# Performance work log

Hardware: AMD Instinct MI355X
Metric: run time of the kernel (lower is better)

## Reference

```python
import jax, jax.numpy as jnp
import numpy as np

HEADS = 16


def setup_inputs() -> dict:
    key = jax.random.key(0)
    ks = jax.random.split(key, 5)
    n, s, d = 2, 2048, 1024
    return {
        "x": jax.random.normal(ks[0], (n, s, d), dtype=jnp.float32),
        "Wqkv": jax.random.normal(ks[1], (3 * d, d), dtype=jnp.float32) * (d ** -0.5),
        "bqkv": jax.random.normal(ks[2], (3 * d,), dtype=jnp.float32) * 0.02,
        "Wd": jax.random.normal(ks[3], (d, d), dtype=jnp.float32) * (d ** -0.5),
        "bd": jax.random.normal(ks[4], (d,), dtype=jnp.float32) * 0.02,
        "mask": 1,
    }


def reference(x, Wqkv, bqkv, Wd, bd, mask):
    n, s, d = x.shape
    h = HEADS
    hd = d // h
    qkv = x @ Wqkv.T + bqkv  # [n, s, 3d]
    q, k, v = jnp.split(qkv, 3, axis=-1)
    # [n, h, s, hd]
    q = q.reshape(n, s, h, hd).transpose(0, 2, 1, 3)
    k = k.reshape(n, s, h, hd).transpose(0, 2, 1, 3)
    v = v.reshape(n, s, h, hd).transpose(0, 2, 1, 3)
    scores = jnp.einsum("bhqd,bhkd->bhqk", q, k)
    if mask:
        causal = jnp.triu(jnp.ones((s, s), dtype=bool), k=1)
        scores = jnp.where(causal, -jnp.inf, scores)
    attn = jax.nn.softmax(scores / jnp.sqrt(jnp.float32(hd)), axis=-1)
    out = jnp.einsum("bhqk,bhkd->bhqd", attn, v)
    out = out.transpose(0, 2, 1, 3).reshape(n, s, d)
    return out @ Wd.T + bd
```

## Files before the change

kernel.cpp:

```cpp
#include <hip/hip_runtime.h>
#include <hip/hip_bf16.h>
#include <cstdint>
#include <cstddef>


typedef __attribute__((ext_vector_type(8))) short bf8_t;
typedef __attribute__((ext_vector_type(4))) float f4_t;

__device__ __forceinline__ unsigned short f2bf(float f) {
    union { float f; unsigned int u; } v; v.f = f;
    unsigned int u = v.u + 0x7FFFu + ((v.u >> 16) & 1u);
    return (unsigned short)(u >> 16);
}
__device__ __forceinline__ float bf2f(unsigned short s) {
    union { unsigned int u; float f; } v; v.u = ((unsigned int)s) << 16;
    return v.f;
}

__device__ __forceinline__ void gl_lds16(const void* g, void* l) {
    __builtin_amdgcn_global_load_lds(
        (const __attribute__((address_space(1))) unsigned int*)g,
        (__attribute__((address_space(3))) unsigned int*)l,
        16, 0, 0);
}

__global__ void cvt_kernel(const float* __restrict__ x,    unsigned short* __restrict__ xb,
                           const float* __restrict__ wq,   unsigned short* __restrict__ wqb,
                           const float* __restrict__ wd,   unsigned short* __restrict__ wdb) {
    int i = blockIdx.x * blockDim.x + threadIdx.x;
    const float* src; unsigned short* dst; int off;
    if (i < 1048576)       { src = x;  dst = xb;  off = i; }
    else if (i < 1835008)  { src = wq; dst = wqb; off = i - 1048576; }
    else                   { src = wd; dst = wdb; off = i - 1835008; }
    float4 f = ((const float4*)src)[off];
    ushort4 o;
    o.x = f2bf(f.x); o.y = f2bf(f.y); o.z = f2bf(f.z); o.w = f2bf(f.w);
    ((ushort4*)dst)[off] = o;
}

template<int MODE, int TM>
__device__ __forceinline__ void gemm_body(
    const unsigned short* __restrict__ A,
    const unsigned short* __restrict__ W,
    const float* __restrict__ bias,
    float* __restrict__ outf,
    unsigned short* __restrict__ qb,
    unsigned short* __restrict__ kb,
    unsigned short* __restrict__ vtb,
    int K, int Nn)
{
    constexpr int HM = TM / 2;
    constexpr int MB = HM / 16;
    constexpr int AI = TM / 32;
    constexpr int SSTG = (TM + 128) * 64;
    constexpr int SMEM = (MODE == 0 && SSTG < 128 * 136) ? 128 * 136 : SSTG;

    __shared__ unsigned short smem[SMEM];
    unsigned short* As = smem;
    unsigned short* Bs = smem + TM * 64;

    const int tid  = threadIdx.x;
    const int lane = tid & 63;
    const int w    = tid >> 6;
    const int wm   = w & 1;
    const int wn   = w >> 1;
    const int quad = lane >> 4;
    const int l16  = lane & 15;
    const int m0   = blockIdx.y * TM;
    const int n0   = blockIdx.x * 128;

    const int lrow = lane >> 3;
    const int lcol = ((lane & 7) ^ lrow) << 3;

    f4_t acc[MB][4];
    {
        f4_t z = {0.f, 0.f, 0.f, 0.f};
        #pragma unroll
        for (int i = 0; i < MB; ++i)
            #pragma unroll
            for (int j = 0; j < 4; ++j) acc[i][j] = z;
    }

    const unsigned short* Agp = A + (size_t)(m0 + w * (TM / 4) + lrow) * K + lcol;
    const unsigned short* Bgp = W + (size_t)(n0 + w * 32 + lrow) * K + lcol;
    unsigned short* lAp = &As[(w * (TM / 4)) * 64];
    unsigned short* lBp = &Bs[(w * 32) * 64];

    for (int kk = 0; kk < K; kk += 64) {
        __syncthreads();
        #pragma unroll
        for (int i = 0; i < AI; ++i)
            gl_lds16(Agp + (size_t)(i * 8) * K + kk, lAp + i * 8 * 64);
        #pragma unroll
        for (int i = 0; i < 4; ++i)
            gl_lds16(Bgp + (size_t)(i * 8) * K + kk, lBp + i * 8 * 64);
        __syncthreads();

        const int sw = l16 & 7;
        #pragma unroll
        for (int ks = 0; ks < 2; ++ks) {
            bf8_t af[MB], bfr[4];
            #pragma unroll
            for (int mb = 0; mb < MB; ++mb)
                af[mb] = *(const bf8_t*)&As[(wm * HM + mb * 16 + l16) * 64 + ((((ks << 2) | quad) ^ sw) << 3)];
            #pragma unroll
            for (int nb = 0; nb < 4; ++nb)
                bfr[nb] = *(const bf8_t*)&Bs[(wn * 64 + nb * 16 + l16) * 64 + ((((ks << 2) | quad) ^ sw) << 3)];
            #pragma unroll
            for (int mb = 0; mb < MB; ++mb)
                #pragma unroll
                for (int nb = 0; nb < 4; ++nb)
                    acc[mb][nb] = __builtin_amdgcn_mfma_f32_16x16x32_bf16(af[mb], bfr[nb], acc[mb][nb], 0, 0, 0);
        }
    }

    if (MODE == 0 && n0 >= 2048) {
        unsigned short* T = smem;
        __syncthreads();
        #pragma unroll
        for (int nb = 0; nb < 4; ++nb) {
            const int colL = wn * 64 + nb * 16 + l16;
            const float bc = bias[n0 + colL];
            #pragma unroll
            for (int mb = 0; mb < MB; ++mb) {
                const int rowL = wm * HM + mb * 16 + quad * 4;
                uint2 p;
                p.x = (unsigned int)f2bf(acc[mb][nb][0] + bc) |
                      ((unsigned int)f2bf(acc[mb][nb][1] + bc) << 16);
                p.y = (unsigned int)f2bf(acc[mb][nb][2] + bc) |
                      ((unsigned int)f2bf(acc[mb][nb][3] + bc) << 16);
                *(uint2*)&T[colL * 136 + rowL] = p;
            }
        }
        __syncthreads();
        const int trow  = tid >> 1;
        const int thalf = (tid & 1) << 6;
        const int head  = ((n0 - 2048) >> 6) + (trow >> 6);
        const int hdi   = trow & 63;
        const int bh    = ((m0 >> 11) << 4) + head;
        const int sq0   = (m0 & 2047) + thalf;
        unsigned short* dst = vtb + ((size_t)bh * 64 + hdi) * 2048 + sq0;
        const unsigned short* srcT = &T[trow * 136 + thalf];
        #pragma unroll
        for (int j = 0; j < 8; ++j)
            *(float4*)(dst + j * 8) = *(const float4*)(srcT + j * 8);
        return;
    }

    #pragma unroll
    for (int nb = 0; nb < 4; ++nb) {
        const int col = n0 + wn * 64 + nb * 16 + l16;
        const float bc = bias[col];
        const int within = col & 1023;
        const int head   = within >> 6;
        const int hdi    = within & 63;
        const bool isQ   = (col < 1024);
        #pragma unroll
        for (int mb = 0; mb < MB; ++mb) {
            #pragma unroll
            for (int r = 0; r < 4; ++r) {
                const int row = m0 + wm * HM + mb * 16 + quad * 4 + r;
                const float v = acc[mb][nb][r] + bc;
                if (MODE == 0) {
                    const int b  = row >> 11;
                    const int sq = row & 2047;
                    const int bh = b * 16 + head;
                    const unsigned short bv = f2bf(v);
                    if (isQ) qb[((size_t)bh * 2048 + sq) * 64 + hdi] = bv;
                    else     kb[((size_t)bh * 2048 + sq) * 64 + hdi] = bv;
                } else {
                    outf[(size_t)row * Nn + col] = v;
                }
            }
        }
    }
}

__global__ __launch_bounds__(256, 2) void qkv_gemm(
    const unsigned short* __restrict__ A, const unsigned short* __restrict__ W,
    const float* __restrict__ bias, unsigned short* __restrict__ qb,
    unsigned short* __restrict__ kb, unsigned short* __restrict__ vtb, int K, int Nn)
{
    gemm_body<0, 128>(A, W, bias, nullptr, qb, kb, vtb, K, Nn);
}

__global__ __launch_bounds__(256, 2) void proj_gemm(
    const unsigned short* __restrict__ A, const unsigned short* __restrict__ W,
    const float* __restrict__ bias, float* __restrict__ outf, int K, int Nn)
{
    gemm_body<1, 64>(A, W, bias, outf, nullptr, nullptr, nullptr, K, Nn);
}

__global__ __launch_bounds__(256, 4) void attn_kernel(
    const unsigned short* __restrict__ qg,
    const unsigned short* __restrict__ kg,
    const unsigned short* __restrict__ vg,
    unsigned short* __restrict__ ao,
    unsigned short* __restrict__ pO,
    float* __restrict__ pL)
{
    __shared__ unsigned short Ks[2][4096];
    __shared__ unsigned short Vs[2][4096];
    __shared__ unsigned short Ps[4096];

    const int tid  = threadIdx.x;
    const int lane = tid & 63;
    const int w    = tid >> 6;
    const int quad = lane >> 4;
    const int l16  = lane & 15;
    const int bx   = blockIdx.x;
    const int bh   = ((bx & 7) << 2) | ((bx >> 3) & 3);
    const int h    = (bx >> 5) & 1;
    const int jj   = bx >> 6;
    const int qtBig   = 31 - jj;
    const int qtSmall = jj;
    const int b    = bh >> 4;
    const int head = bh & 15;
    const int p0len = 32 - jj;
    const int t0 = h ? 17 : 0;
    const int t1 = h ? 33 : 17;

    const unsigned short* Qp = qg + (size_t)bh * 2048 * 64;
    const unsigned short* Kp = kg + (size_t)bh * 2048 * 64;
    const unsigned short* Vp = vg + (size_t)bh * 64 * 2048;

    const int srow = lane >> 3;
    const int scol = ((lane & 7) ^ srow) << 3;
    const unsigned short* kga = Kp + (size_t)(w * 16 + srow) * 64 + scol;
    const unsigned short* vga = Vp + (size_t)(w * 16 + srow) * 2048 + scol;
    const int sw = l16 & 7;

    auto stageKV = [&](int kt, int buf) {
        const int sk0 = kt << 6;
        gl_lds16(kga + (size_t)sk0 * 64,       &Ks[buf][w * 16 * 64]);
        gl_lds16(kga + (size_t)sk0 * 64 + 512, &Ks[buf][(w * 16 + 8) * 64]);
        gl_lds16(vga + sk0,                    &Vs[buf][w * 16 * 64]);
        gl_lds16(vga + sk0 + 8 * 2048,         &Vs[buf][(w * 16 + 8) * 64]);
    };

    bf8_t bones;
    {
        const short one = (l16 == 0) ? (short)0x3F80 : (short)0;
        #pragma unroll
        for (int j = 0; j < 8; ++j) bones[j] = one;
    }

    f4_t oacc[4];
    f4_t lacc;
    {
        f4_t z = {0.f, 0.f, 0.f, 0.f};
        #pragma unroll
        for (int j = 0; j < 4; ++j) oacc[j] = z;
        lacc = z;
    }

    bf8_t aq[2];
    {
        const int qt_init = (t0 >= p0len) ? qtSmall : qtBig;
        const size_t qrow = (size_t)(qt_init * 64 + w * 16 + l16) * 64;
        aq[0] = *(const bf8_t*)(Qp + qrow + quad * 8);
        aq[1] = *(const bf8_t*)(Qp + qrow + 32 + quad * 8);
    }

    auto flushPartial = [&]() {
        const int tb = (h << 9) + (bh << 4) + jj;
        unsigned short* po = pO + (size_t)tb * 4096;
        #pragma unroll
        for (int r = 0; r < 4; ++r) {
            const int row = w * 16 + quad * 4 + r;
            #pragma unroll
            for (int nb = 0; nb < 4; ++nb)
                po[row * 64 + nb * 16 + l16] = f2bf(oacc[nb][r]);
            if (l16 == 0) pL[tb * 64 + row] = lacc[r];
        }
    };

    {
        const int kt0 = (t0 >= p0len) ? (t0 - p0len) : t0;
        stageKV(kt0, t0 & 1);
    }

    for (int t = t0; t < t1; ++t) {
        const int buf = t & 1;
        __syncthreads();

        if (t + 1 < t1) {
            const int t2 = t + 1;
            stageKV((t2 >= p0len) ? (t2 - p0len) : t2, t2 & 1);
        }

        if (t == p0len) {
            flushPartial();
            f4_t z = {0.f, 0.f, 0.f, 0.f};
            #pragma unroll
            for (int j = 0; j < 4; ++j) oacc[j] = z;
            lacc = z;
            const size_t qrow = (size_t)(qtSmall * 64 + w * 16 + l16) * 64;
            aq[0] = *(const bf8_t*)(Qp + qrow + quad * 8);
            aq[1] = *(const bf8_t*)(Qp + qrow + 32 + quad * 8);
        }

        const bool ph1 = (t >= p0len);
        const int  kt  = ph1 ? (t - p0len) : t;
        const int  qtc = ph1 ? qtSmall : qtBig;
        const bool diag = (kt == qtc);

        f4_t sacc[4];
        {
            f4_t z = {0.f, 0.f, 0.f, 0.f};
            #pragma unroll
            for (int j = 0; j < 4; ++j) sacc[j] = z;
        }
        __builtin_amdgcn_s_setprio(1);
        #pragma unroll
        for (int ks = 0; ks < 2; ++ks) {
            #pragma unroll
            for (int nb = 0; nb < 4; ++nb) {
                bf8_t bk = *(const bf8_t*)&Ks[buf][(nb * 16 + l16) * 64 + ((((ks << 2) | quad) ^ sw) << 3)];
                sacc[nb] = __builtin_amdgcn_mfma_f32_16x16x32_bf16(aq[ks], bk, sacc[nb], 0, 0, 0);
            }
        }
        __builtin_amdgcn_s_setprio(0);

        if (!diag) {
            #pragma unroll
            for (int r = 0; r < 4; ++r) {
                const int rloc = (w << 4) + (quad << 2) + r;
                const int rk = rloc & 7;
                #pragma unroll
                for (int nb = 0; nb < 4; ++nb) {
                    union { float f; unsigned int u; } pv;
                    pv.f = exp2f(fmaf(sacc[nb][r], 0.18033688f, -20.197731f));
                    Ps[rloc * 64 + ((((nb << 1) | (l16 >> 3)) ^ rk) << 3) + (l16 & 7)] =
                        (unsigned short)(pv.u >> 16);
                }
            }
        } else {
            #pragma unroll
            for (int r = 0; r < 4; ++r) {
                const int rloc = (w << 4) + (quad << 2) + r;
                const int rk = rloc & 7;
                #pragma unroll
                for (int nb = 0; nb < 4; ++nb) {
                    float e = fmaf(sacc[nb][r], 0.18033688f, -20.197731f);
                    if (nb * 16 + l16 > rloc) e = -1e30f;
                    union { float f; unsigned int u; } pv;
                    pv.f = exp2f(e);
                    Ps[rloc * 64 + ((((nb << 1) | (l16 >> 3)) ^ rk) << 3) + (l16 & 7)] =
                        (unsigned short)(pv.u >> 16);
                }
            }
        }

        __builtin_amdgcn_s_setprio(1);
        #pragma unroll
        for (int ks = 0; ks < 2; ++ks) {
            bf8_t ap = *(const bf8_t*)&Ps[(w * 16 + l16) * 64 + ((((ks << 2) | quad) ^ sw) << 3)];
            #pragma unroll
            for (int nb = 0; nb < 4; ++nb) {
                bf8_t bv = *(const bf8_t*)&Vs[buf][(nb * 16 + l16) * 64 + ((((ks << 2) | quad) ^ sw) << 3)];
                oacc[nb] = __builtin_amdgcn_mfma_f32_16x16x32_bf16(ap, bv, oacc[nb], 0, 0, 0);
            }
            lacc = __builtin_amdgcn_mfma_f32_16x16x32_bf16(ap, bones, lacc, 0, 0, 0);
        }
        __builtin_amdgcn_s_setprio(0);
    }

    if (!h) {
        flushPartial();
    } else {
        #pragma unroll
        for (int r = 0; r < 4; ++r) {
            const float lsum = __shfl(lacc[r], lane & 48);
            const float rl = 1.f / lsum;
            const int sq = qtSmall * 64 + (w << 4) + (quad << 2) + r;
            #pragma unroll
            for (int nb = 0; nb < 4; ++nb) {
                const int dcol = head * 64 + nb * 16 + l16;
                ao[((size_t)(b * 2048 + sq)) * 1024 + dcol] = f2bf(oacc[nb][r] * rl);
            }
        }
    }
}

__global__ void merge_kernel(const unsigned short* __restrict__ pO,
                             const float* __restrict__ pL,
                             unsigned short* __restrict__ ao) {
    const int blk  = blockIdx.x;
    const int bh   = blk >> 4;
    const int jj   = blk & 15;
    const int b    = bh >> 4;
    const int head = bh & 15;
    const int qt   = 31 - jj;
    const int row  = threadIdx.x >> 2;
    const int c0   = (threadIdx.x & 3) << 4;

    const float l = pL[blk * 64 + row] + pL[(512 + blk) * 64 + row];
    const float rl = 1.f / l;
    const unsigned short* p0 = pO + (size_t)blk * 4096 + row * 64 + c0;
    const unsigned short* p1 = pO + (size_t)(512 + blk) * 4096 + row * 64 + c0;
    unsigned short* dst = ao + ((size_t)(b * 2048 + qt * 64 + row)) * 1024 + head * 64 + c0;
    #pragma unroll
    for (int j = 0; j < 16; ++j)
        dst[j] = f2bf((bf2f(p0[j]) + bf2f(p1[j])) * rl);
}

extern "C" void kernel_launch(void* const* d_in, const int* in_sizes, int n_in,
                              void* d_out, int out_size, void* d_ws, size_t ws_size,
                              hipStream_t stream) {
    const float* x    = (const float*)d_in[0];
    const float* Wqkv = (const float*)d_in[1];
    const float* bqkv = (const float*)d_in[2];
    const float* Wd   = (const float*)d_in[3];
    const float* bd   = (const float*)d_in[4];
    float* out = (float*)d_out;

    char* ws = (char*)d_ws;
    unsigned short* xb    = (unsigned short*)(ws);
    unsigned short* wqkvb = (unsigned short*)(ws + 8388608);
    unsigned short* wdb   = (unsigned short*)(ws + 14680064);
    unsigned short* qb2   = (unsigned short*)(ws + 16777216);
    unsigned short* kb2   = (unsigned short*)(ws + 25165824);
    unsigned short* vtb   = (unsigned short*)(ws + 33554432);
    unsigned short* pO    = (unsigned short*)(ws + 41943040);
    float*          pL    = (float*)(ws + 50331648);
    unsigned short* ao    = xb;

    cvt_kernel<<<8192, 256, 0, stream>>>(x, xb, Wqkv, wqkvb, Wd, wdb);

    qkv_gemm<<<dim3(24, 32), 256, 0, stream>>>(
        xb, wqkvb, bqkv, qb2, kb2, vtb, 1024, 3072);

    attn_kernel<<<1024, 256, 0, stream>>>(qb2, kb2, vtb, ao, pO, pL);

    merge_kernel<<<512, 256, 0, stream>>>(pO, pL, ao);

    proj_gemm<<<dim3(8, 64), 256, 0, stream>>>(
        ao, wdb, bd, out, 1024, 1024);
}
```

Baseline: 175.0 us.

## Replace split-KV balanced attention with one block per query tile, drop merge

Each of the 1024 attention blocks used to pair a long and a short causal query tile and split the combined key range into two halves, writing bf16 partials that a separate merge kernel combined. Now each block owns one query tile (qt = 31 - bx>>5) and loops over keys 0..qt, normalizing and writing output directly. This removes the merge launch and the partial-result traffic. In exchange, per-block work becomes imbalanced (1 to 32 key tiles), with the heaviest tiles scheduled first to soften the tail.

```diff
diff --git a/kernel.cpp b/kernel.cpp
--- a/kernel.cpp
+++ b/kernel.cpp
@@ -195,9 +195,7 @@
     const unsigned short* __restrict__ qg,
     const unsigned short* __restrict__ kg,
     const unsigned short* __restrict__ vg,
-    unsigned short* __restrict__ ao,
-    unsigned short* __restrict__ pO,
-    float* __restrict__ pL)
+    unsigned short* __restrict__ ao)
 {
     __shared__ unsigned short Ks[2][4096];
     __shared__ unsigned short Vs[2][4096];
@@ -210,15 +208,9 @@
     const int l16  = lane & 15;
     const int bx   = blockIdx.x;
     const int bh   = ((bx & 7) << 2) | ((bx >> 3) & 3);
-    const int h    = (bx >> 5) & 1;
-    const int jj   = bx >> 6;
-    const int qtBig   = 31 - jj;
-    const int qtSmall = jj;
+    const int qt   = 31 - (bx >> 5);
     const int b    = bh >> 4;
     const int head = bh & 15;
-    const int p0len = 32 - jj;
-    const int t0 = h ? 17 : 0;
-    const int t1 = h ? 33 : 17;
 
     const unsigned short* Qp = qg + (size_t)bh * 2048 * 64;
     const unsigned short* Kp = kg + (size_t)bh * 2048 * 64;
@@ -256,54 +248,21 @@
 
     bf8_t aq[2];
     {
-        const int qt_init = (t0 >= p0len) ? qtSmall : qtBig;
-        const size_t qrow = (size_t)(qt_init * 64 + w * 16 + l16) * 64;
+        const size_t qrow = (size_t)(qt * 64 + w * 16 + l16) * 64;
         aq[0] = *(const bf8_t*)(Qp + qrow + quad * 8);
         aq[1] = *(const bf8_t*)(Qp + qrow + 32 + quad * 8);
     }
 
-    auto flushPartial = [&]() {
-        const int tb = (h << 9) + (bh << 4) + jj;
-        unsigned short* po = pO + (size_t)tb * 4096;
-        #pragma unroll
-        for (int r = 0; r < 4; ++r) {
-            const int row = w * 16 + quad * 4 + r;
-            #pragma unroll
-            for (int nb = 0; nb < 4; ++nb)
-                po[row * 64 + nb * 16 + l16] = f2bf(oacc[nb][r]);
-            if (l16 == 0) pL[tb * 64 + row] = lacc[r];
-        }
-    };
-
-    {
-        const int kt0 = (t0 >= p0len) ? (t0 - p0len) : t0;
-        stageKV(kt0, t0 & 1);
-    }
-
-    for (int t = t0; t < t1; ++t) {
+    stageKV(0, 0);
+
+    for (int t = 0; t <= qt; ++t) {
         const int buf = t & 1;
         __syncthreads();
 
-        if (t + 1 < t1) {
-            const int t2 = t + 1;
-            stageKV((t2 >= p0len) ? (t2 - p0len) : t2, t2 & 1);
-        }
-
-        if (t == p0len) {
-            flushPartial();
-            f4_t z = {0.f, 0.f, 0.f, 0.f};
-            #pragma unroll
-            for (int j = 0; j < 4; ++j) oacc[j] = z;
-            lacc = z;
-            const size_t qrow = (size_t)(qtSmall * 64 + w * 16 + l16) * 64;
-            aq[0] = *(const bf8_t*)(Qp + qrow + quad * 8);
-            aq[1] = *(const bf8_t*)(Qp + qrow + 32 + quad * 8);
-        }
-
-        const bool ph1 = (t >= p0len);
-        const int  kt  = ph1 ? (t - p0len) : t;
-        const int  qtc = ph1 ? qtSmall : qtBig;
-        const bool diag = (kt == qtc);
+        if (t < qt)
+            stageKV(t + 1, (t + 1) & 1);
+
+        const bool diag = (t == qt);
 
         f4_t sacc[4];
         {
@@ -366,43 +325,17 @@
         __builtin_amdgcn_s_setprio(0);
     }
 
-    if (!h) {
-        flushPartial();
-    } else {
-        #pragma unroll
-        for (int r = 0; r < 4; ++r) {
-            const float lsum = __shfl(lacc[r], lane & 48);
-            const float rl = 1.f / lsum;
-            const int sq = qtSmall * 64 + (w << 4) + (quad << 2) + r;
-            #pragma unroll
-            for (int nb = 0; nb < 4; ++nb) {
-                const int dcol = head * 64 + nb * 16 + l16;
-                ao[((size_t)(b * 2048 + sq)) * 1024 + dcol] = f2bf(oacc[nb][r] * rl);
-            }
-        }
-    }
-}
-
-__global__ void merge_kernel(const unsigned short* __restrict__ pO,
-                             const float* __restrict__ pL,
-                             unsigned short* __restrict__ ao) {
-    const int blk  = blockIdx.x;
-    const int bh   = blk >> 4;
-    const int jj   = blk & 15;
-    const int b    = bh >> 4;
-    const int head = bh & 15;
-    const int qt   = 31 - jj;
-    const int row  = threadIdx.x >> 2;
-    const int c0   = (threadIdx.x & 3) << 4;
-
-    const float l = pL[blk * 64 + row] + pL[(512 + blk) * 64 + row];
-    const float rl = 1.f / l;
-    const unsigned short* p0 = pO + (size_t)blk * 4096 + row * 64 + c0;
-    const unsigned short* p1 = pO + (size_t)(512 + blk) * 4096 + row * 64 + c0;
-    unsigned short* dst = ao + ((size_t)(b * 2048 + qt * 64 + row)) * 1024 + head * 64 + c0;
     #pragma unroll
-    for (int j = 0; j < 16; ++j)
-        dst[j] = f2bf((bf2f(p0[j]) + bf2f(p1[j])) * rl);
+    for (int r = 0; r < 4; ++r) {
+        const float lsum = __shfl(lacc[r], lane & 48);
+        const float rl = 1.f / lsum;
+        const int sq = qt * 64 + (w << 4) + (quad << 2) + r;
+        #pragma unroll
+        for (int nb = 0; nb < 4; ++nb) {
+            const int dcol = head * 64 + nb * 16 + l16;
+            ao[((size_t)(b * 2048 + sq)) * 1024 + dcol] = f2bf(oacc[nb][r] * rl);
+        }
+    }
 }
 
 extern "C" void kernel_launch(void* const* d_in, const int* in_sizes, int n_in,
@@ -422,8 +355,6 @@
     unsigned short* qb2   = (unsigned short*)(ws + 16777216);
     unsigned short* kb2   = (unsigned short*)(ws + 25165824);
     unsigned short* vtb   = (unsigned short*)(ws + 33554432);
-    unsigned short* pO    = (unsigned short*)(ws + 41943040);
-    float*          pL    = (float*)(ws + 50331648);
     unsigned short* ao    = xb;
 
     cvt_kernel<<<8192, 256, 0, stream>>>(x, xb, Wqkv, wqkvb, Wd, wdb);
@@ -431,9 +362,7 @@
     qkv_gemm<<<dim3(24, 32), 256, 0, stream>>>(
         xb, wqkvb, bqkv, qb2, kb2, vtb, 1024, 3072);
 
-    attn_kernel<<<1024, 256, 0, stream>>>(qb2, kb2, vtb, ao, pO, pL);
-
-    merge_kernel<<<512, 256, 0, stream>>>(pO, pL, ao);
+    attn_kernel<<<1024, 256, 0, stream>>>(qb2, kb2, vtb, ao);
 
     proj_gemm<<<dim3(8, 64), 256, 0, stream>>>(
         ao, wdb, bd, out, 1024, 1024);
```

New measurement: 178.3 us. Within noise of the previous version (+1.9%).

## Fuse split-K attention merge into attention kernel via atomic pair counter

Applied to the files above, without the earlier changes.

Removes the separate merge kernel launch. The last-arriving of the two blocks that share a query tile now merges the two partial results itself, using an atomic counter per tile that the conversion kernel zeroes. This saves one launch and the global round-trip tail of the merge kernel. In exchange it adds threadfences, extra syncthreads and an atomic in the attention kernel, and the merge work now sits on the critical path of some attention blocks.

```diff
diff --git a/kernel.cpp b/kernel.cpp
--- a/kernel.cpp
+++ b/kernel.cpp
@@ -26,7 +26,12 @@
 
 __global__ void cvt_kernel(const float* __restrict__ x,    unsigned short* __restrict__ xb,
                            const float* __restrict__ wq,   unsigned short* __restrict__ wqb,
-                           const float* __restrict__ wd,   unsigned short* __restrict__ wdb) {
+                           const float* __restrict__ wd,   unsigned short* __restrict__ wdb,
+                           int* __restrict__ cnt) {
+    if (blockIdx.x == 0) {
+        cnt[threadIdx.x] = 0;
+        cnt[threadIdx.x + 256] = 0;
+    }
     int i = blockIdx.x * blockDim.x + threadIdx.x;
     const float* src; unsigned short* dst; int off;
     if (i < 1048576)       { src = x;  dst = xb;  off = i; }
@@ -197,7 +202,8 @@
     const unsigned short* __restrict__ vg,
     unsigned short* __restrict__ ao,
     unsigned short* __restrict__ pO,
-    float* __restrict__ pL)
+    float* __restrict__ pL,
+    int* __restrict__ cnt)
 {
     __shared__ unsigned short Ks[2][4096];
     __shared__ unsigned short Vs[2][4096];
@@ -219,6 +225,7 @@
     const int p0len = 32 - jj;
     const int t0 = h ? 17 : 0;
     const int t1 = h ? 33 : 17;
+    const int pair = (bh << 4) + jj;
 
     const unsigned short* Qp = qg + (size_t)bh * 2048 * 64;
     const unsigned short* Kp = kg + (size_t)bh * 2048 * 64;
@@ -263,7 +270,7 @@
     }
 
     auto flushPartial = [&]() {
-        const int tb = (h << 9) + (bh << 4) + jj;
+        const int tb = (h << 9) + pair;
         unsigned short* po = pO + (size_t)tb * 4096;
         #pragma unroll
         for (int r = 0; r < 4; ++r) {
@@ -275,6 +282,28 @@
         }
     };
 
+    auto mergeIfSecond = [&]() {
+        __threadfence();
+        __syncthreads();
+        if (tid == 0)
+            Ps[0] = (atomicAdd(&cnt[pair], 1) == 1) ? (unsigned short)1 : (unsigned short)0;
+        __syncthreads();
+        const bool second = (Ps[0] != 0);
+        if (second) {
+            __threadfence();
+            const int row = tid >> 2;
+            const int c0  = (tid & 3) << 4;
+            const float l = pL[pair * 64 + row] + pL[(512 + pair) * 64 + row];
+            const float rl = 1.f / l;
+            const unsigned short* p0 = pO + (size_t)pair * 4096 + row * 64 + c0;
+            const unsigned short* p1 = pO + (size_t)(512 + pair) * 4096 + row * 64 + c0;
+            unsigned short* dst = ao + ((size_t)(b * 2048 + qtBig * 64 + row)) * 1024 + head * 64 + c0;
+            #pragma unroll
+            for (int j = 0; j < 16; ++j)
+                dst[j] = f2bf((bf2f(p0[j]) + bf2f(p1[j])) * rl);
+        }
+    };
+
     {
         const int kt0 = (t0 >= p0len) ? (t0 - p0len) : t0;
         stageKV(kt0, t0 & 1);
@@ -291,6 +320,7 @@
 
         if (t == p0len) {
             flushPartial();
+            mergeIfSecond();
             f4_t z = {0.f, 0.f, 0.f, 0.f};
             #pragma unroll
             for (int j = 0; j < 4; ++j) oacc[j] = z;
@@ -368,6 +398,7 @@
 
     if (!h) {
         flushPartial();
+        mergeIfSecond();
     } else {
         #pragma unroll
         for (int r = 0; r < 4; ++r) {
@@ -381,28 +412,6 @@
             }
         }
     }
-}
-
-__global__ void merge_kernel(const unsigned short* __restrict__ pO,
-                             const float* __restrict__ pL,
-                             unsigned short* __restrict__ ao) {
-    const int blk  = blockIdx.x;
-    const int bh   = blk >> 4;
-    const int jj   = blk & 15;
-    const int b    = bh >> 4;
-    const int head = bh & 15;
-    const int qt   = 31 - jj;
-    const int row  = threadIdx.x >> 2;
-    const int c0   = (threadIdx.x & 3) << 4;
-
-    const float l = pL[blk * 64 + row] + pL[(512 + blk) * 64 + row];
-    const float rl = 1.f / l;
-    const unsigned short* p0 = pO + (size_t)blk * 4096 + row * 64 + c0;
-    const unsigned short* p1 = pO + (size_t)(512 + blk) * 4096 + row * 64 + c0;
-    unsigned short* dst = ao + ((size_t)(b * 2048 + qt * 64 + row)) * 1024 + head * 64 + c0;
-    #pragma unroll
-    for (int j = 0; j < 16; ++j)
-        dst[j] = f2bf((bf2f(p0[j]) + bf2f(p1[j])) * rl);
 }
 
 extern "C" void kernel_launch(void* const* d_in, const int* in_sizes, int n_in,
@@ -424,16 +433,15 @@
     unsigned short* vtb   = (unsigned short*)(ws + 33554432);
     unsigned short* pO    = (unsigned short*)(ws + 41943040);
     float*          pL    = (float*)(ws + 50331648);
+    int*            cnt   = (int*)(ws + 50593792);
     unsigned short* ao    = xb;
 
-    cvt_kernel<<<8192, 256, 0, stream>>>(x, xb, Wqkv, wqkvb, Wd, wdb);
+    cvt_kernel<<<8192, 256, 0, stream>>>(x, xb, Wqkv, wqkvb, Wd, wdb, cnt);
 
     qkv_gemm<<<dim3(24, 32), 256, 0, stream>>>(
         xb, wqkvb, bqkv, qb2, kb2, vtb, 1024, 3072);
 
-    attn_kernel<<<1024, 256, 0, stream>>>(qb2, kb2, vtb, ao, pO, pL);
-
-    merge_kernel<<<512, 256, 0, stream>>>(pO, pL, ao);
+    attn_kernel<<<1024, 256, 0, stream>>>(qb2, kb2, vtb, ao, pO, pL, cnt);
 
     proj_gemm<<<dim3(8, 64), 256, 0, stream>>>(
         ao, wdb, bd, out, 1024, 1024);
```

Measured after the change: 350.8 us. 2x slower.

## Read V directly from global memory and transpose S MFMA for packed P stores

Applied to the files above, without the earlier changes.

V tiles are no longer staged into LDS. Each wave now loads its V fragments straight from global memory inside the PV loop, which removes the V LDS buffers and their async copies. The QK^T MFMA swaps its operands so each lane holds four consecutive keys of one query row, letting probabilities be packed and written to LDS as 8-byte stores instead of scalar 2-byte writes. The cost is global loads of V that are not prefetched and sit on the critical path (mostly L2 hits). In exchange, LDS use drops, which may raise occupancy.

```diff
diff --git a/kernel.cpp b/kernel.cpp
--- a/kernel.cpp
+++ b/kernel.cpp
@@ -200,7 +200,6 @@
     float* __restrict__ pL)
 {
     __shared__ unsigned short Ks[2][4096];
-    __shared__ unsigned short Vs[2][4096];
     __shared__ unsigned short Ps[4096];
 
     const int tid  = threadIdx.x;
@@ -227,15 +226,12 @@
     const int srow = lane >> 3;
     const int scol = ((lane & 7) ^ srow) << 3;
     const unsigned short* kga = Kp + (size_t)(w * 16 + srow) * 64 + scol;
-    const unsigned short* vga = Vp + (size_t)(w * 16 + srow) * 2048 + scol;
     const int sw = l16 & 7;
 
-    auto stageKV = [&](int kt, int buf) {
+    auto stageK = [&](int kt, int buf) {
         const int sk0 = kt << 6;
         gl_lds16(kga + (size_t)sk0 * 64,       &Ks[buf][w * 16 * 64]);
         gl_lds16(kga + (size_t)sk0 * 64 + 512, &Ks[buf][(w * 16 + 8) * 64]);
-        gl_lds16(vga + sk0,                    &Vs[buf][w * 16 * 64]);
-        gl_lds16(vga + sk0 + 8 * 2048,         &Vs[buf][(w * 16 + 8) * 64]);
     };
 
     bf8_t bones;
@@ -257,9 +253,9 @@
     bf8_t aq[2];
     {
         const int qt_init = (t0 >= p0len) ? qtSmall : qtBig;
-        const size_t qrow = (size_t)(qt_init * 64 + w * 16 + l16) * 64;
-        aq[0] = *(const bf8_t*)(Qp + qrow + quad * 8);
-        aq[1] = *(const bf8_t*)(Qp + qrow + 32 + quad * 8);
+        const size_t qrow0 = (size_t)(qt_init * 64 + w * 16 + l16) * 64;
+        aq[0] = *(const bf8_t*)(Qp + qrow0 + quad * 8);
+        aq[1] = *(const bf8_t*)(Qp + qrow0 + 32 + quad * 8);
     }
 
     auto flushPartial = [&]() {
@@ -277,8 +273,12 @@
 
     {
         const int kt0 = (t0 >= p0len) ? (t0 - p0len) : t0;
-        stageKV(kt0, t0 & 1);
-    }
+        stageK(kt0, t0 & 1);
+    }
+
+    const int qrow = (w << 4) + l16;
+    const int qk8  = l16 & 7;
+    const unsigned short* vb = Vp + (size_t)l16 * 2048;
 
     for (int t = t0; t < t1; ++t) {
         const int buf = t & 1;
@@ -286,7 +286,7 @@
 
         if (t + 1 < t1) {
             const int t2 = t + 1;
-            stageKV((t2 >= p0len) ? (t2 - p0len) : t2, t2 & 1);
+            stageK((t2 >= p0len) ? (t2 - p0len) : t2, t2 & 1);
         }
 
         if (t == p0len) {
@@ -295,15 +295,16 @@
             #pragma unroll
             for (int j = 0; j < 4; ++j) oacc[j] = z;
             lacc = z;
-            const size_t qrow = (size_t)(qtSmall * 64 + w * 16 + l16) * 64;
-            aq[0] = *(const bf8_t*)(Qp + qrow + quad * 8);
-            aq[1] = *(const bf8_t*)(Qp + qrow + 32 + quad * 8);
+            const size_t qrow2 = (size_t)(qtSmall * 64 + w * 16 + l16) * 64;
+            aq[0] = *(const bf8_t*)(Qp + qrow2 + quad * 8);
+            aq[1] = *(const bf8_t*)(Qp + qrow2 + 32 + quad * 8);
         }
 
         const bool ph1 = (t >= p0len);
         const int  kt  = ph1 ? (t - p0len) : t;
         const int  qtc = ph1 ? qtSmall : qtBig;
         const bool diag = (kt == qtc);
+        const int  sk0 = kt << 6;
 
         f4_t sacc[4];
         {
@@ -317,38 +318,38 @@
             #pragma unroll
             for (int nb = 0; nb < 4; ++nb) {
                 bf8_t bk = *(const bf8_t*)&Ks[buf][(nb * 16 + l16) * 64 + ((((ks << 2) | quad) ^ sw) << 3)];
-                sacc[nb] = __builtin_amdgcn_mfma_f32_16x16x32_bf16(aq[ks], bk, sacc[nb], 0, 0, 0);
+                sacc[nb] = __builtin_amdgcn_mfma_f32_16x16x32_bf16(bk, aq[ks], sacc[nb], 0, 0, 0);
             }
         }
         __builtin_amdgcn_s_setprio(0);
 
         if (!diag) {
             #pragma unroll
-            for (int r = 0; r < 4; ++r) {
-                const int rloc = (w << 4) + (quad << 2) + r;
-                const int rk = rloc & 7;
+            for (int nb = 0; nb < 4; ++nb) {
+                union { float f; unsigned int u; } p0v, p1v, p2v, p3v;
+                p0v.f = exp2f(fmaf(sacc[nb][0], 0.18033688f, -20.197731f));
+                p1v.f = exp2f(fmaf(sacc[nb][1], 0.18033688f, -20.197731f));
+                p2v.f = exp2f(fmaf(sacc[nb][2], 0.18033688f, -20.197731f));
+                p3v.f = exp2f(fmaf(sacc[nb][3], 0.18033688f, -20.197731f));
+                uint2 pk;
+                pk.x = (p0v.u >> 16) | (p1v.u & 0xFFFF0000u);
+                pk.y = (p2v.u >> 16) | (p3v.u & 0xFFFF0000u);
+                *(uint2*)&Ps[qrow * 64 + ((((nb << 1) | (quad >> 1)) ^ qk8) << 3) + ((quad & 1) << 2)] = pk;
+            }
+        } else {
+            #pragma unroll
+            for (int nb = 0; nb < 4; ++nb) {
+                union { float f; unsigned int u; } pv[4];
                 #pragma unroll
-                for (int nb = 0; nb < 4; ++nb) {
-                    union { float f; unsigned int u; } pv;
-                    pv.f = exp2f(fmaf(sacc[nb][r], 0.18033688f, -20.197731f));
-                    Ps[rloc * 64 + ((((nb << 1) | (l16 >> 3)) ^ rk) << 3) + (l16 & 7)] =
-                        (unsigned short)(pv.u >> 16);
+                for (int r = 0; r < 4; ++r) {
+                    float e = fmaf(sacc[nb][r], 0.18033688f, -20.197731f);
+                    if ((nb << 4) + (quad << 2) + r > qrow) e = -1e30f;
+                    pv[r].f = exp2f(e);
                 }
-            }
-        } else {
-            #pragma unroll
-            for (int r = 0; r < 4; ++r) {
-                const int rloc = (w << 4) + (quad << 2) + r;
-                const int rk = rloc & 7;
-                #pragma unroll
-                for (int nb = 0; nb < 4; ++nb) {
-                    float e = fmaf(sacc[nb][r], 0.18033688f, -20.197731f);
-                    if (nb * 16 + l16 > rloc) e = -1e30f;
-                    union { float f; unsigned int u; } pv;
-                    pv.f = exp2f(e);
-                    Ps[rloc * 64 + ((((nb << 1) | (l16 >> 3)) ^ rk) << 3) + (l16 & 7)] =
-                        (unsigned short)(pv.u >> 16);
-                }
+                uint2 pk;
+                pk.x = (pv[0].u >> 16) | (pv[1].u & 0xFFFF0000u);
+                pk.y = (pv[2].u >> 16) | (pv[3].u & 0xFFFF0000u);
+                *(uint2*)&Ps[qrow * 64 + ((((nb << 1) | (quad >> 1)) ^ qk8) << 3) + ((quad & 1) << 2)] = pk;
             }
         }
 
@@ -358,7 +359,7 @@
             bf8_t ap = *(const bf8_t*)&Ps[(w * 16 + l16) * 64 + ((((ks << 2) | quad) ^ sw) << 3)];
             #pragma unroll
             for (int nb = 0; nb < 4; ++nb) {
-                bf8_t bv = *(const bf8_t*)&Vs[buf][(nb * 16 + l16) * 64 + ((((ks << 2) | quad) ^ sw) << 3)];
+                bf8_t bv = *(const bf8_t*)(vb + (size_t)(nb * 16) * 2048 + sk0 + (((ks << 2) | quad) << 3));
                 oacc[nb] = __builtin_amdgcn_mfma_f32_16x16x32_bf16(ap, bv, oacc[nb], 0, 0, 0);
             }
             lacc = __builtin_amdgcn_mfma_f32_16x16x32_bf16(ap, bones, lacc, 0, 0, 0);
```

Measured after the change: 205.6 us. 1.17x slower.
